# Optimization experiments

Hardware: AMD Instinct MI355X
Metric: run time of the kernel (lower is better)

## Reference

```python
import jax, jax.numpy as jnp
import numpy as np

# Model constants (match init_kwargs + mamba_ssm defaults)
CIN, COUT, K, STRIDE = 64, 128, 4, 4
D = 128            # d_model = features_out
DI = 256           # d_inner = 2*D (expand=2)
NSTATE = 16        # d_state
DCONV = 4          # depthwise conv width
DT_RANK = 8        # ceil(D/16)
NB = 3             # blocks per direction
NTOT = 2 * NB      # forward + backward stacks


def setup_inputs() -> dict:
    key = jax.random.key(0)
    ks = jax.random.split(key, 10)
    s = 0.02
    x = jax.random.normal(ks[0], (2, CIN, 8192), jnp.float32)
    convd_w = jax.random.normal(ks[1], (COUT, CIN, K), jnp.float32) * s
    convd_b = jnp.zeros((COUT,), jnp.float32)
    ln_w = jnp.ones((NTOT, D), jnp.float32)
    ln_b = jnp.zeros((NTOT, D), jnp.float32)
    in_proj_w = jax.random.normal(ks[2], (NTOT, 2 * DI, D), jnp.float32) * s
    conv_w = jax.random.normal(ks[3], (NTOT, DI, DCONV), jnp.float32) * s
    conv_b = jnp.zeros((NTOT, DI), jnp.float32)
    xproj_w = jax.random.normal(ks[4], (NTOT, DT_RANK + 2 * NSTATE, DI), jnp.float32) * s
    dtproj_w = jax.random.normal(ks[5], (NTOT, DI, DT_RANK), jnp.float32) * s
    dtproj_b = jax.random.normal(ks[6], (NTOT, DI), jnp.float32) * s
    # S4D-real init: A = -[1..N]
    A_log = jnp.log(jnp.broadcast_to(jnp.arange(1, NSTATE + 1, dtype=jnp.float32), (NTOT, DI, NSTATE)))
    Dparam = jnp.ones((NTOT, DI), jnp.float32)
    outproj_w = jax.random.normal(ks[7], (NTOT, D, DI), jnp.float32) * s
    return dict(x=x, convd_w=convd_w, convd_b=convd_b, ln_w=ln_w, ln_b=ln_b,
                in_proj_w=in_proj_w, conv_w=conv_w, conv_b=conv_b, xproj_w=xproj_w,
                dtproj_w=dtproj_w, dtproj_b=dtproj_b, A_log=A_log, Dparam=Dparam,
                outproj_w=outproj_w)


def _silu(x):
    return x * jax.nn.sigmoid(x)


def _layernorm(x, w, b, eps=1e-5):
    m = x.mean(-1, keepdims=True)
    xc = x - m
    v = (xc * xc).mean(-1, keepdims=True)
    return xc * jax.lax.rsqrt(v + eps) * w + b


def _mamba_mixer(x, in_proj_w, conv_w, conv_b, xproj_w, dtproj_w, dtproj_b, A_log, Dp, outproj_w):
    # x: (B, L, D)
    B, L, _ = x.shape
    xz = jnp.einsum('bld,ed->ble', x, in_proj_w)          # (B, L, 2*DI)
    xm, z = jnp.split(xz, 2, axis=-1)
    # causal depthwise conv (pad left DCONV-1, truncate to L)
    xp = jnp.pad(xm, ((0, 0), (DCONV - 1, 0), (0, 0)))
    xc = conv_b
    acc = jnp.zeros_like(xm)
    for k in range(DCONV):
        acc = acc + xp[:, k:k + L, :] * conv_w[:, k]
    xc = _silu(acc + conv_b)                               # (B, L, DI)
    dbc = jnp.einsum('ble,ne->bln', xc, xproj_w)           # (B, L, DT_RANK + 2N)
    dt, Bc, Cc = jnp.split(dbc, [DT_RANK, DT_RANK + NSTATE], axis=-1)
    dt = jax.nn.softplus(jnp.einsum('blr,dr->bld', dt, dtproj_w) + dtproj_b)  # (B, L, DI)
    A = -jnp.exp(A_log)                                    # (DI, N)
    dA = jnp.exp(dt[..., None] * A)                        # (B, L, DI, N)
    dBx = dt[..., None] * Bc[:, :, None, :] * xc[..., None]

    def step(h, inp):
        dA_t, dBx_t, C_t = inp
        h = dA_t * h + dBx_t                               # (B, DI, N)
        y = jnp.einsum('bdn,bn->bd', h, C_t)
        return h, y

    h0 = jnp.zeros((B, DI, NSTATE), x.dtype)
    _, ys = jax.lax.scan(step, h0, (jnp.swapaxes(dA, 0, 1), jnp.swapaxes(dBx, 0, 1), jnp.swapaxes(Cc, 0, 1)))
    y = jnp.swapaxes(ys, 0, 1)                             # (B, L, DI)
    y = (y + Dp * xc) * _silu(z)
    return jnp.einsum('ble,de->bld', y, outproj_w)         # (B, L, D)


def _mamba_stack(x, off, ln_w, ln_b, in_proj_w, conv_w, conv_b, xproj_w, dtproj_w, dtproj_b, A_log, Dparam, outproj_w):
    # mamba_ssm Block semantics: residual = x (+ prev residual); x = mixer(norm(residual))
    res = None
    cur = x
    for i in range(NB):
        j = off + i
        res = cur if res is None else cur + res
        hn = _layernorm(res, ln_w[j], ln_b[j])
        cur = _mamba_mixer(hn, in_proj_w[j], conv_w[j], conv_b[j], xproj_w[j],
                           dtproj_w[j], dtproj_b[j], A_log[j], Dparam[j], outproj_w[j])
    return cur, res


def reference(x, convd_w, convd_b, ln_w, ln_b, in_proj_w, conv_w, conv_b, xproj_w,
              dtproj_w, dtproj_b, A_log, Dparam, outproj_w):
    # downsampling conv + SiLU
    y = jax.lax.conv_general_dilated(x, convd_w, (STRIDE,), 'VALID',
                                     dimension_numbers=('NCH', 'OIH', 'NCH'))
    y = _silu(y + convd_b[None, :, None])                  # (B, COUT, L')
    h = jnp.swapaxes(y, 1, 2)                              # (B, L', D)
    xf, rf = _mamba_stack(h, 0, ln_w, ln_b, in_proj_w, conv_w, conv_b, xproj_w,
                          dtproj_w, dtproj_b, A_log, Dparam, outproj_w)
    xb, rb = _mamba_stack(h[:, ::-1, :], NB, ln_w, ln_b, in_proj_w, conv_w, conv_b, xproj_w,
                          dtproj_w, dtproj_b, A_log, Dparam, outproj_w)
    out = (xf + rf) + (xb + rb)[:, ::-1, :]
    return jnp.swapaxes(out, 1, 2), rf, rb
```

## Files before the change

### kernel.cpp

```cpp
#include <hip/hip_runtime.h>
#include <math.h>

#define B    2
#define CIN  64
#define LIN  8192
#define L    2048
#define D    128
#define DI   256
#define NS   16
#define RK   8
#define NSTREAM 4
#define CH   32
#define NCH  (L/CH)
#define TOK  (NSTREAM*L)
#define SZ_D ((size_t)TOK*D)
#define SZ_DI ((size_t)TOK*DI)
#define SXM 280
#define SHN 152

typedef short  bfrag __attribute__((ext_vector_type(8)));
typedef float  facc  __attribute__((ext_vector_type(4)));
#define MFMA __builtin_amdgcn_mfma_f32_16x16x32_bf16

__device__ __forceinline__ float sigmoidf_(float x){ return 1.f/(1.f+__expf(-x)); }
__device__ __forceinline__ float siluf_(float x){ return x*sigmoidf_(x); }
__device__ __forceinline__ ushort f2bf(float f){
    unsigned u = __float_as_uint(f);
    u += 0x7fffu + ((u>>16)&1u);
    return (ushort)(u>>16);
}
__device__ __forceinline__ float bf2f(ushort u){ return __uint_as_float(((unsigned)u)<<16); }
__device__ __forceinline__ float softplusf_(float t){
    return (t > 20.f) ? t : __logf(1.f + __expf(t));
}

__global__ void __launch_bounds__(256,1)
k_downcvt(const float* __restrict__ x, const float* __restrict__ convd_w,
          const float* __restrict__ bias,
          const float* __restrict__ ipw, const float* __restrict__ opw,
          const float* __restrict__ xpw,
          float* __restrict__ h, ushort* __restrict__ wall){
    int tid = threadIdx.x;
    if (blockIdx.x >= 128){
        int g = (blockIdx.x - 128)*256 + tid;
        for (int i = g; i < 688128; i += 32768){
// ... 30 lines not shown
    __syncthreads();
    int w = tid>>6, lane = tid&63, rw = w>>1, cw_ = w&1;
    int q = lane>>4, r = lane&15;
    int n0 = nb*64 + cw_*32;
    facc acc[2][2] = {};
    #pragma unroll
    for (int kb=0; kb<8; ++kb){
        bfrag a0 = *(bfrag*)&sxd[(rw*32 + r)*SXM + kb*32 + q*8];
        bfrag a1 = *(bfrag*)&sxd[(rw*32 + 16 + r)*SXM + kb*32 + q*8];
        bfrag b0 = *(bfrag*)&swt[(cw_*32 + r)*SXM + kb*32 + q*8];
        bfrag b1 = *(bfrag*)&swt[(cw_*32 + 16 + r)*SXM + kb*32 + q*8];
        acc[0][0] = MFMA(a0,b0,acc[0][0],0,0,0);
        acc[0][1] = MFMA(a0,b1,acc[0][1],0,0,0);
        acc[1][0] = MFMA(a1,b0,acc[1][0],0,0,0);
        acc[1][1] = MFMA(a1,b1,acc[1][1],0,0,0);
    }
    #pragma unroll
    for (int im=0; im<2; ++im)
    #pragma unroll
    for (int in=0; in<2; ++in){
        int col = n0 + in*16 + r;
        float bv = bias[col];
        #pragma unroll
        for (int r2=0; r2<4; ++r2){
            int row = m0 + rw*32 + im*16 + q*4 + r2;
            int bb = row >> 11, l = row & 2047;
            float v = siluf_(acc[im][in][r2] + bv);
            h[((size_t)(bb*L + l))*D + col] = v;
            h[((size_t)((2+bb)*L + (L-1-l)))*D + col] = v;
        }
    }
}

__global__ void __launch_bounds__(512,1)
k_head(const float* __restrict__ curIn, const float* __restrict__ resIn,
       float* __restrict__ resOut,
       const float* __restrict__ lnw, const float* __restrict__ lnb,
       const ushort* __restrict__ wbi, const ushort* __restrict__ wbx,
       const float* __restrict__ cw, const float* __restrict__ cb,
       const float* __restrict__ Wdt, const float* __restrict__ bdt,
       const float* __restrict__ A_log,
       ushort* __restrict__ zh, ushort* __restrict__ xch,
       float* __restrict__ dtr, float* __restrict__ Bc, float* __restrict__ Cc,
       float* __restrict__ Aprod, float* __restrict__ Bend, int blk, int first){
    __shared__ ushort smHn[35*SHN];
    __shared__ ushort smXm[35*SXM];
    __shared__ ushort smXc[32*SXM];
    __shared__ float  smDbc[32*68];
    const int tid = threadIdx.x;
    const int bi = blockIdx.x;
    const int s = bi >> 6, c = bi & 63;
    const int j = (s>>1)*3 + blk;
    const int base_tok = s*L + c*CH;

    {
        int t = tid >> 4, g = tid & 15;
        size_t off = (size_t)(base_tok + t)*D + g*8;
        float4 v[2];
        const float4* cp = (const float4*)(curIn + off);
        v[0] = cp[0]; v[1] = cp[1];
        if (!first){
            const float4* rp = (const float4*)(resIn + off);
            #pragma unroll
            for (int i=0;i<2;++i){ float4 rv=rp[i]; v[i].x+=rv.x; v[i].y+=rv.y; v[i].z+=rv.z; v[i].w+=rv.w; }
        }
        {
            float4* ro = (float4*)(resOut + off);
            ro[0] = v[0]; ro[1] = v[1];
        }
        float s1=0.f, s2=0.f;
        #pragma unroll
        for (int i=0;i<2;++i){
            s1 += v[i].x+v[i].y+v[i].z+v[i].w;
            s2 += v[i].x*v[i].x+v[i].y*v[i].y+v[i].z*v[i].z+v[i].w*v[i].w;
        }
        s1 += __shfl_xor(s1,1); s2 += __shfl_xor(s2,1);
        s1 += __shfl_xor(s1,2); s2 += __shfl_xor(s2,2);
        s1 += __shfl_xor(s1,4); s2 += __shfl_xor(s2,4);
        s1 += __shfl_xor(s1,8); s2 += __shfl_xor(s2,8);
        float mean = s1*(1.f/128.f);
        float var  = s2*(1.f/128.f) - mean*mean;
        float rstd = rsqrtf(var + 1e-5f);
        const float4* lwp = (const float4*)(lnw + j*D + g*8);
        const float4* lbp = (const float4*)(lnb + j*D + g*8);
        #pragma unroll
        for (int i=0;i<2;++i){
            float4 lw = lwp[i], lb = lbp[i];
            ushort4 o;
            o.x = f2bf((v[i].x-mean)*rstd*lw.x + lb.x);
            o.y = f2bf((v[i].y-mean)*rstd*lw.y + lb.y);
            o.z = f2bf((v[i].z-mean)*rstd*lw.z + lb.z);
            o.w = f2bf((v[i].w-mean)*rstd*lw.w + lb.w);
            *(ushort4*)&smHn[t*SHN + g*8 + i*4] = o;
        }
    }
    if (c > 0 && tid < 48){
        int t = tid >> 4, g = tid & 15;
        size_t off = (size_t)(base_tok - 3 + t)*D + g*8;
        float4 v[2];
        const float4* cp = (const float4*)(curIn + off);
        v[0] = cp[0]; v[1] = cp[1];
        if (!first){
            const float4* rp = (const float4*)(resIn + off);
            #pragma unroll
            for (int i=0;i<2;++i){ float4 rv=rp[i]; v[i].x+=rv.x; v[i].y+=rv.y; v[i].z+=rv.z; v[i].w+=rv.w; }
        }
        float s1=0.f, s2=0.f;
        #pragma unroll
        for (int i=0;i<2;++i){
            s1 += v[i].x+v[i].y+v[i].z+v[i].w;
            s2 += v[i].x*v[i].x+v[i].y*v[i].y+v[i].z*v[i].z+v[i].w*v[i].w;
        }
        s1 += __shfl_xor(s1,1); s2 += __shfl_xor(s2,1);
        s1 += __shfl_xor(s1,2); s2 += __shfl_xor(s2,2);
        s1 += __shfl_xor(s1,4); s2 += __shfl_xor(s2,4);
        s1 += __shfl_xor(s1,8); s2 += __shfl_xor(s2,8);
        float mean = s1*(1.f/128.f);
        float var  = s2*(1.f/128.f) - mean*mean;
        float rstd = rsqrtf(var + 1e-5f);
        const float4* lwp = (const float4*)(lnw + j*D + g*8);
        const float4* lbp = (const float4*)(lnb + j*D + g*8);
        #pragma unroll
        for (int i=0;i<2;++i){
            float4 lw = lwp[i], lb = lbp[i];
            ushort4 o;
            o.x = f2bf((v[i].x-mean)*rstd*lw.x + lb.x);
            o.y = f2bf((v[i].y-mean)*rstd*lw.y + lb.y);
            o.z = f2bf((v[i].z-mean)*rstd*lw.z + lb.z);
            o.w = f2bf((v[i].w-mean)*rstd*lw.w + lb.w);
            *(ushort4*)&smHn[(32+t)*SHN + g*8 + i*4] = o;
        }
    }
    __syncthreads();

    {
        int w = tid>>6, lane = tid&63, q = lane>>4, r = lane&15;
        bfrag a[3][4];
        #pragma unroll
        for (int rt=0; rt<3; ++rt)
        #pragma unroll
        for (int kb=0; kb<4; ++kb)
            a[rt][kb] = *(bfrag*)&smHn[(rt*16 + r)*SHN + kb*32 + q*8];
        #pragma unroll
        for (int ct=0; ct<4; ++ct){
            int n0 = w*64 + ct*16;
            const ushort* bp = wbi + ((size_t)j*512 + n0 + r)*128 + q*8;
            facc a0 = {}, a1 = {}, a2 = {};
            #pragma unroll
            for (int kb=0; kb<4; ++kb){
                bfrag bv = *(const bfrag*)(bp + kb*32);
                a0 = MFMA(a[0][kb], bv, a0, 0,0,0);
                a1 = MFMA(a[1][kb], bv, a1, 0,0,0);
                a2 = MFMA(a[2][kb], bv, a2, 0,0,0);
            }
            int colL = n0 + r;
            if (colL < DI){
                #pragma unroll
                for (int r2=0;r2<4;++r2){
                    int rr = q*4 + r2;
                    smXm[rr*SXM + colL]      = f2bf(a0[r2]);
                    smXm[(16+rr)*SXM + colL] = f2bf(a1[r2]);
                    if (rr < 3) smXm[(32+rr)*SXM + colL] = f2bf(a2[r2]);
                }
            } else {
                int cz = colL - DI;
                #pragma unroll
                for (int r2=0;r2<4;++r2){
                    int rr = q*4 + r2;
                    zh[(size_t)(base_tok + rr)*DI + cz]      = f2bf(a0[r2]);
                    zh[(size_t)(base_tok + 16 + rr)*DI + cz] = f2bf(a1[r2]);
                }
            }
        }
    }
    __syncthreads();

    {
        int d = tid & 255, th = tid >> 8;
        const float* w4 = cw + ((size_t)j*DI + d)*4;
        float cw0=w4[0], cw1=w4[1], cw2=w4[2], cw3=w4[3];
        float cbb = cb[j*DI + d];
        float xm1, xm2, xm3;
        if (th == 0){
            xm1 = xm2 = xm3 = 0.f;
            if (c > 0){
                xm3 = bf2f(smXm[32*SXM + d]);
                xm2 = bf2f(smXm[33*SXM + d]);
                xm1 = bf2f(smXm[34*SXM + d]);
            }
        } else {
            xm3 = bf2f(smXm[13*SXM + d]);
            xm2 = bf2f(smXm[14*SXM + d]);
            xm1 = bf2f(smXm[15*SXM + d]);
        }
        int l0 = th*16;
        #pragma unroll 4
        for (int i=0;i<16;++i){
            int l = l0 + i;
            float x0 = bf2f(smXm[l*SXM + d]);
            float v = siluf_(cbb + cw3*x0 + cw2*xm1 + cw1*xm2 + cw0*xm3);
            ushort vb = f2bf(v);
            smXc[l*SXM + d] = vb;
            xch[(size_t)(base_tok+l)*DI + d] = vb;
            xm3 = xm2; xm2 = xm1; xm1 = x0;
        }
    }
    __syncthreads();

    if (tid < 256){
        int w = tid>>6, lane = tid&63, q = lane>>4, r = lane&15;
        facc a0 = {}, a1 = {};
        const ushort* bp = wbx + ((size_t)j*64 + w*16 + r)*256 + q*8;
        #pragma unroll
        for (int kb=0; kb<8; ++kb){
            bfrag av0 = *(bfrag*)&smXc[r*SXM + kb*32 + q*8];
            bfrag av1 = *(bfrag*)&smXc[(16+r)*SXM + kb*32 + q*8];
            bfrag bv  = *(const bfrag*)(bp + kb*32);
            a0 = MFMA(av0, bv, a0, 0,0,0);
            a1 = MFMA(av1, bv, a1, 0,0,0);
        }
        int col = w*16 + r;
        #pragma unroll
        for (int r2=0;r2<4;++r2){
            int rr = q*4 + r2;
            smDbc[rr*68 + col]      = a0[r2];
            smDbc[(16+rr)*68 + col] = a1[r2];
            int row0 = base_tok + rr, row1 = base_tok + 16 + rr;
            if      (col < 8){  dtr[(size_t)row0*RK + col] = a0[r2];      dtr[(size_t)row1*RK + col] = a1[r2]; }
            else if (col < 24){ Bc [(size_t)row0*NS + (col-8)] = a0[r2];  Bc [(size_t)row1*NS + (col-8)] = a1[r2]; }
            else if (col < 40){ Cc [(size_t)row0*NS + (col-24)] = a0[r2]; Cc [(size_t)row1*NS + (col-24)] = a1[r2]; }
        }
    }
    __syncthreads();

    {
        int d = tid & 255, hh = tid >> 8;
        float A[8], wv[RK];
        const float* ar = A_log + ((size_t)j*DI + d)*NS + hh*8;
        #pragma unroll
        for (int n=0;n<8;++n) A[n] = -__expf(ar[n]);
        const float* wr = Wdt + ((size_t)j*DI + d)*RK;
        #pragma unroll
        for (int r=0;r<RK;++r) wv[r] = wr[r];
        float bb2 = bdt[j*DI + d];
        float ap[8], hs[8];
        #pragma unroll
        for (int n=0;n<8;++n){ ap[n]=1.f; hs[n]=0.f; }
        #pragma unroll 4
        for (int l=0;l<CH;++l){
            float t = bb2;
            #pragma unroll
            for (int r=0;r<RK;++r) t += smDbc[l*68+r]*wv[r];
            float dtv = softplusf_(t);
            float xv  = bf2f(smXc[l*SXM + d]);
            float dbx = dtv*xv;
            #pragma unroll
            for (int n=0;n<8;++n){
                float dA = __expf(dtv*A[n]);
                ap[n] *= dA;
                hs[n] = dA*hs[n] + dbx*smDbc[l*68+8+hh*8+n];
            }
        }
        size_t pb = (size_t)bi*4096 + (size_t)d*16 + hh*8;
        #pragma unroll
        for (int k4=0;k4<2;++k4){
            float4 av, bv;
            av.x=ap[k4*4+0]; av.y=ap[k4*4+1]; av.z=ap[k4*4+2]; av.w=ap[k4*4+3];
            bv.x=hs[k4*4+0]; bv.y=hs[k4*4+1]; bv.z=hs[k4*4+2]; bv.w=hs[k4*4+3];
            *(float4*)&Aprod[pb + k4*4] = av;
            *(float4*)&Bend [pb + k4*4] = bv;
        }
    }
}

__global__ void k_scanmid(const float* __restrict__ Aprod, float* __restrict__ Bend){
    int tid = blockIdx.x*128 + threadIdx.x;
    int s = tid >> 12;
    int nd = tid & 4095;
    size_t base = (size_t)s*NCH*4096 + nd;
    float h = 0.f;
    for (int c0=0; c0<NCH; c0+=16){
        float a[16], b[16];
        #pragma unroll
        for (int i=0;i<16;++i){
            a[i] = Aprod[base + (size_t)(c0+i)*4096];
            b[i] = Bend [base + (size_t)(c0+i)*4096];
        }
        #pragma unroll
        for (int i=0;i<16;++i){
            Bend[base + (size_t)(c0+i)*4096] = h;
            h = a[i]*h + b[i];
        }
    }
}

__global__ void __launch_bounds__(512,1)
k_tail(const float* __restrict__ dtr, const ushort* __restrict__ xch,
       const float* __restrict__ Bc, const float* __restrict__ Cc,
       const float* __restrict__ A_log,
       const float* __restrict__ Wdt, const float* __restrict__ bdt,
       const float* __restrict__ h0, const ushort* __restrict__ zh,
       const float* __restrict__ Dp, const ushort* __restrict__ wbo,
       float* __restrict__ cur, int blk){
    int c = blockIdx.x, s = blockIdx.y; int j = (s>>1)*3 + blk;
    int tid = threadIdx.x;
    __shared__ float sB[CH*NS], sC[CH*NS], sdtr[CH*RK];
    __shared__ ushort sg[CH*SXM];
    int base_tok = s*L + c*CH;
    sB[tid] = Bc[(size_t)base_tok*NS + tid];
    sC[tid] = Cc[(size_t)base_tok*NS + tid];
    if (tid < 256) sdtr[tid] = dtr[(size_t)base_tok*RK + tid];
    int d = tid >> 1, hh = tid & 1;
    float A[8], wv[RK];
    const float* ar = A_log + ((size_t)j*DI + d)*NS + hh*8;
    #pragma unroll
    for (int n=0;n<8;++n) A[n] = -__expf(ar[n]);
    const float* wr = Wdt + ((size_t)j*DI + d)*RK;
    #pragma unroll
    for (int r=0;r<RK;++r) wv[r] = wr[r];
    float bb = bdt[j*DI + d];
    float Dpd = Dp[j*DI + d];
    float hs[8];
    {
        size_t pb = (size_t)(s*NCH + c)*4096 + (size_t)d*16 + hh*8;
        float4 h0v0 = *(const float4*)&h0[pb];
        float4 h0v1 = *(const float4*)&h0[pb+4];
        hs[0]=h0v0.x; hs[1]=h0v0.y; hs[2]=h0v0.z; hs[3]=h0v0.w;
        hs[4]=h0v1.x; hs[5]=h0v1.y; hs[6]=h0v1.z; hs[7]=h0v1.w;
    }
    __syncthreads();
    #pragma unroll 4
    for (int l=0;l<CH;++l){
        float t = bb;
        #pragma unroll
        for (int r=0;r<RK;++r) t += sdtr[l*RK+r]*wv[r];
        float dtv = softplusf_(t);
        float xv  = bf2f(xch[(size_t)(base_tok+l)*DI + d]);
        float dbx = dtv*xv;
        float p = 0.f;
        #pragma unroll
        for (int n=0;n<8;++n){
            float dA = __expf(dtv*A[n]);
            hs[n] = dA*hs[n] + dbx*sB[l*NS+hh*8+n];
            p += hs[n]*sC[l*NS+hh*8+n];
        }
        p += __shfl_xor(p, 1);
        if (hh == 0){
            float zv = bf2f(zh[(size_t)(base_tok+l)*DI + d]);
            sg[l*SXM + d] = f2bf((p + Dpd*xv)*siluf_(zv));
        }
    }
    __syncthreads();
    int w = tid>>6, lane = tid&63, q = lane>>4, r = lane&15;
    facc acc0 = {}, acc1 = {};
    const ushort* b0p = wbo + ((size_t)j*128 + w*16 + r)*256 + q*8;
    #pragma unroll
    for (int kb=0; kb<8; ++kb){
        bfrag av0 = *(bfrag*)&sg[r*SXM + kb*32 + q*8];
        bfrag av1 = *(bfrag*)&sg[(16+r)*SXM + kb*32 + q*8];
        bfrag bv0 = *(const bfrag*)(b0p + kb*32);
        acc0 = MFMA(av0,bv0,acc0,0,0,0);
        acc1 = MFMA(av1,bv0,acc1,0,0,0);
    }
    int col = w*16 + r;
    #pragma unroll
    for (int r2=0;r2<4;++r2){
        int row0 = base_tok + q*4 + r2;
        cur[(size_t)row0*D + col]      = acc0[r2];
        cur[(size_t)(row0+16)*D + col] = acc1[r2];
    }
}

__global__ void k_final(const float* __restrict__ cur, const float* __restrict__ res,
                        float* __restrict__ out){
    int l = blockIdx.x, b = blockIdx.y, d = threadIdx.x;
    int tf = (b*L + l)*D + d;
    int tbk = ((2+b)*L + (L-1-l))*D + d;
    float f  = cur[tf] + res[tf];
    float bw = cur[tbk] + res[tbk];
    out[((size_t)(b*D + d))*L + l] = f + bw;
    out[(size_t)2*D*L + (size_t)(b*L + l)*D + d] = res[tf];
    out[(size_t)2*D*L + (size_t)((2+b)*L + l)*D + d] = res[((2+b)*L + l)*D + d];
}

extern "C" void kernel_launch(void* const* d_in, const int* in_sizes, int n_in,
                              void* d_out, int out_size, void* d_ws, size_t ws_size,
                              hipStream_t stream){
    const float* x         = (const float*)d_in[0];
    const float* convd_w   = (const float*)d_in[1];
    const float* convd_b   = (const float*)d_in[2];
    const float* ln_w      = (const float*)d_in[3];
    const float* ln_b      = (const float*)d_in[4];
    const float* in_proj_w = (const float*)d_in[5];
    const float* conv_w    = (const float*)d_in[6];
    const float* conv_b    = (const float*)d_in[7];
    const float* xproj_w   = (const float*)d_in[8];
    const float* dtproj_w  = (const float*)d_in[9];
    const float* dtproj_b  = (const float*)d_in[10];
    const float* A_log     = (const float*)d_in[11];
    const float* Dparam    = (const float*)d_in[12];
    const float* outproj_w = (const float*)d_in[13];

    float* ws = (float*)d_ws;
    float* h     = ws; ws += SZ_D;
    float* res0  = ws; ws += SZ_D;
    float* res1  = ws; ws += SZ_D;
    float* cur   = ws; ws += SZ_D;
    ushort* zh   = (ushort*)ws; ws += SZ_DI/2;
    ushort* xch  = (ushort*)ws; ws += SZ_DI/2;
    float* Aprod = ws; ws += SZ_D;
    float* Bend  = ws; ws += SZ_D;
    float* dtr   = ws; ws += (size_t)TOK*RK;
    float* Bc    = ws; ws += (size_t)TOK*NS;
    float* Cc    = ws; ws += (size_t)TOK*NS;
    ushort* wall = (ushort*)ws;
    ushort* wbi  = wall;
    ushort* wbo  = wall + 393216;
    ushort* wbx  = wall + 589824;

    k_downcvt<<<256, 256, 0, stream>>>(x, convd_w, convd_b, in_proj_w, outproj_w,
                                       xproj_w, h, wall);

    float* resin[3]  = { nullptr, res0, res1 };
    float* resout[3] = { res0,    res1, res0 };
    for (int blk = 0; blk < 3; ++blk){
        const float* ci = (blk==0) ? h : cur;
        const float* ri = (blk==0) ? h : resin[blk];
        k_head<<<NSTREAM*NCH, 512, 0, stream>>>(ci, ri, resout[blk], ln_w, ln_b, wbi, wbx,
                                                conv_w, conv_b, dtproj_w, dtproj_b, A_log,
                                                zh, xch, dtr, Bc, Cc, Aprod, Bend, blk, blk==0);
        k_scanmid<<<128, 128, 0, stream>>>(Aprod, Bend);
        k_tail<<<dim3(NCH, NSTREAM), 512, 0, stream>>>(dtr, xch, Bc, Cc, A_log,
                                                       dtproj_w, dtproj_b, Bend, zh,
                                                       Dparam, wbo, cur, blk);
    }

    k_final<<<dim3(L, B), 128, 0, stream>>>(cur, res0, (float*)d_out);
}
```

Baseline: 264.8 us.

## Fuse head, chunk scan and tail into one kernel with inter-block lookback flags

Merges the per-layer head, mid-scan and tail kernels into a single kernel where each chunk block publishes its chunk-local decay product and end state, waits on flags for earlier chunks, and serially combines their prefixes to get its initial state. This removes two launches per layer and the global round trips for xc, dt, B and C intermediates, keeping them in shared memory. It relies on all blocks being co-resident for the spin-wait and adds a lookback whose cost grows with the chunk index. The final output kernel also transposes through shared memory for coalesced stores.

After: 351.8 us. 32.8% more time.

```diff
diff --git a/kernel.cpp b/kernel.cpp
--- a/kernel.cpp
+++ b/kernel.cpp
@@ -108,22 +108,26 @@
 }
 
 __global__ void __launch_bounds__(512,1)
-k_head(const float* __restrict__ curIn, const float* __restrict__ resIn,
-       float* __restrict__ resOut,
-       const float* __restrict__ lnw, const float* __restrict__ lnb,
-       const ushort* __restrict__ wbi, const ushort* __restrict__ wbx,
-       const float* __restrict__ cw, const float* __restrict__ cb,
-       const float* __restrict__ Wdt, const float* __restrict__ bdt,
-       const float* __restrict__ A_log,
-       ushort* __restrict__ zh, ushort* __restrict__ xch,
-       float* __restrict__ dtr, float* __restrict__ Bc, float* __restrict__ Cc,
-       float* __restrict__ Aprod, float* __restrict__ Bend, int blk, int first){
-    __shared__ ushort smHn[35*SHN];
-    __shared__ ushort smXm[35*SXM];
-    __shared__ ushort smXc[32*SXM];
-    __shared__ float  smDbc[32*68];
+k_layer(const float* __restrict__ curIn, const float* __restrict__ resIn,
+        float* __restrict__ resOut, float* __restrict__ curOut,
+        const float* __restrict__ lnw, const float* __restrict__ lnb,
+        const ushort* __restrict__ wbi, const ushort* __restrict__ wbx,
+        const ushort* __restrict__ wbo,
+        const float* __restrict__ cw, const float* __restrict__ cb,
+        const float* __restrict__ Wdt, const float* __restrict__ bdt,
+        const float* __restrict__ A_log, const float* __restrict__ Dp,
+        ushort* __restrict__ zh,
+        float* __restrict__ Ap, float* __restrict__ Bp,
+        unsigned* __restrict__ fl, int blk, int first){
+    __shared__ __align__(16) char smem[56864];
+    ushort* smHn  = (ushort*)smem;
+    ushort* smXm  = (ushort*)(smem + 10640);
+    ushort* smXc  = (ushort*)(smem + 30240);
+    float*  smDbc = (float*) (smem + 48160);
+    ushort* sg    = (ushort*)smem;
+
     const int tid = threadIdx.x;
-    const int bi = blockIdx.x;
+    const int bi  = blockIdx.x;
     const int s = bi >> 6, c = bi & 63;
     const int j = (s>>1)*3 + blk;
     const int base_tok = s*L + c*CH;
@@ -274,9 +278,7 @@
             int l = l0 + i;
             float x0 = bf2f(smXm[l*SXM + d]);
             float v = siluf_(cbb + cw3*x0 + cw2*xm1 + cw1*xm2 + cw0*xm3);
-            ushort vb = f2bf(v);
-            smXc[l*SXM + d] = vb;
-            xch[(size_t)(base_tok+l)*DI + d] = vb;
+            smXc[l*SXM + d] = f2bf(v);
             xm3 = xm2; xm2 = xm1; xm1 = x0;
         }
     }
@@ -300,162 +302,173 @@
             int rr = q*4 + r2;
             smDbc[rr*68 + col]      = a0[r2];
             smDbc[(16+rr)*68 + col] = a1[r2];
-            int row0 = base_tok + rr, row1 = base_tok + 16 + rr;
-            if      (col < 8){  dtr[(size_t)row0*RK + col] = a0[r2];      dtr[(size_t)row1*RK + col] = a1[r2]; }
-            else if (col < 24){ Bc [(size_t)row0*NS + (col-8)] = a0[r2];  Bc [(size_t)row1*NS + (col-8)] = a1[r2]; }
-            else if (col < 40){ Cc [(size_t)row0*NS + (col-24)] = a0[r2]; Cc [(size_t)row1*NS + (col-24)] = a1[r2]; }
-        }
-    }
-    __syncthreads();
-
-    {
-        int d = tid & 255, hh = tid >> 8;
-        float A[8], wv[RK];
-        const float* ar = A_log + ((size_t)j*DI + d)*NS + hh*8;
-        #pragma unroll
-        for (int n=0;n<8;++n) A[n] = -__expf(ar[n]);
-        const float* wr = Wdt + ((size_t)j*DI + d)*RK;
+        }
+    }
+    __syncthreads();
+
+    const int d2 = tid >> 1, hh = tid & 1;
+    float A8[8], wv[RK];
+    {
+        const float* ar = A_log + ((size_t)j*DI + d2)*NS + hh*8;
+        #pragma unroll
+        for (int n=0;n<8;++n) A8[n] = -__expf(ar[n]);
+        const float* wr = Wdt + ((size_t)j*DI + d2)*RK;
         #pragma unroll
         for (int r=0;r<RK;++r) wv[r] = wr[r];
-        float bb2 = bdt[j*DI + d];
-        float ap[8], hs[8];
-        #pragma unroll
-        for (int n=0;n<8;++n){ ap[n]=1.f; hs[n]=0.f; }
+    }
+    const float bb2 = bdt[j*DI + d2];
+
+    {
+        float ap[8], hsv[8];
+        #pragma unroll
+        for (int n=0;n<8;++n){ ap[n]=1.f; hsv[n]=0.f; }
         #pragma unroll 4
         for (int l=0;l<CH;++l){
             float t = bb2;
             #pragma unroll
             for (int r=0;r<RK;++r) t += smDbc[l*68+r]*wv[r];
             float dtv = softplusf_(t);
-            float xv  = bf2f(smXc[l*SXM + d]);
+            float xv  = bf2f(smXc[l*SXM + d2]);
             float dbx = dtv*xv;
             #pragma unroll
             for (int n=0;n<8;++n){
-                float dA = __expf(dtv*A[n]);
+                float dA = __expf(dtv*A8[n]);
                 ap[n] *= dA;
+                hsv[n] = dA*hsv[n] + dbx*smDbc[l*68+8+hh*8+n];
+            }
+        }
+        size_t pb = (size_t)bi*4096 + (size_t)d2*16 + hh*8;
+        float4 av0, av1, bv0, bv1;
+        av0.x=ap[0];av0.y=ap[1];av0.z=ap[2];av0.w=ap[3];
+        av1.x=ap[4];av1.y=ap[5];av1.z=ap[6];av1.w=ap[7];
+        bv0.x=hsv[0];bv0.y=hsv[1];bv0.z=hsv[2];bv0.w=hsv[3];
+        bv1.x=hsv[4];bv1.y=hsv[5];bv1.z=hsv[6];bv1.w=hsv[7];
+        *(float4*)&Ap[pb]   = av0; *(float4*)&Ap[pb+4] = av1;
+        *(float4*)&Bp[pb]   = bv0; *(float4*)&Bp[pb+4] = bv1;
+    }
+    __syncthreads();
+    if (tid == 0){
+        __threadfence();
+        __hip_atomic_store(&fl[bi], 1u, __ATOMIC_RELEASE, __HIP_MEMORY_SCOPE_AGENT);
+    }
+    if (tid < 64 && c > 0){
+        const unsigned* fp = fl + s*64 + tid;
+        bool ok = (tid >= c);
+        unsigned guard = 0;
+        while (true){
+            if (!ok) ok = (__hip_atomic_load(fp, __ATOMIC_ACQUIRE, __HIP_MEMORY_SCOPE_AGENT) != 0);
+            if (__all(ok)) break;
+            __builtin_amdgcn_s_sleep(2);
+            if (++guard > 20000000u) break;
+        }
+    }
+    __syncthreads();
+
+    float hs[8];
+    #pragma unroll
+    for (int n=0;n<8;++n) hs[n] = 0.f;
+    {
+        size_t sb = ((size_t)(s*64))*4096 + (size_t)d2*16 + hh*8;
+        int ci = 0;
+        for (; ci+4 <= c; ci += 4){
+            float4 aa[4][2], bb4[4][2];
+            #pragma unroll
+            for (int u=0;u<4;++u){
+                const float4* av = (const float4*)&Ap[sb + (size_t)(ci+u)*4096];
+                const float4* bv = (const float4*)&Bp[sb + (size_t)(ci+u)*4096];
+                aa[u][0]=av[0]; aa[u][1]=av[1]; bb4[u][0]=bv[0]; bb4[u][1]=bv[1];
+            }
+            #pragma unroll
+            for (int u=0;u<4;++u){
+                hs[0]=aa[u][0].x*hs[0]+bb4[u][0].x; hs[1]=aa[u][0].y*hs[1]+bb4[u][0].y;
+                hs[2]=aa[u][0].z*hs[2]+bb4[u][0].z; hs[3]=aa[u][0].w*hs[3]+bb4[u][0].w;
+                hs[4]=aa[u][1].x*hs[4]+bb4[u][1].x; hs[5]=aa[u][1].y*hs[5]+bb4[u][1].y;
+                hs[6]=aa[u][1].z*hs[6]+bb4[u][1].z; hs[7]=aa[u][1].w*hs[7]+bb4[u][1].w;
+            }
+        }
+        for (; ci < c; ++ci){
+            const float4* av = (const float4*)&Ap[sb + (size_t)ci*4096];
+            const float4* bv = (const float4*)&Bp[sb + (size_t)ci*4096];
+            float4 a0=av[0], a1=av[1], b0=bv[0], b1=bv[1];
+            hs[0]=a0.x*hs[0]+b0.x; hs[1]=a0.y*hs[1]+b0.y;
+            hs[2]=a0.z*hs[2]+b0.z; hs[3]=a0.w*hs[3]+b0.w;
+            hs[4]=a1.x*hs[4]+b1.x; hs[5]=a1.y*hs[5]+b1.y;
+            hs[6]=a1.z*hs[6]+b1.z; hs[7]=a1.w*hs[7]+b1.w;
+        }
+    }
+
+    {
+        float Dpd = Dp[j*DI + d2];
+        #pragma unroll 4
+        for (int l=0;l<CH;++l){
+            float t = bb2;
+            #pragma unroll
+            for (int r=0;r<RK;++r) t += smDbc[l*68+r]*wv[r];
+            float dtv = softplusf_(t);
+            float xv  = bf2f(smXc[l*SXM + d2]);
+            float dbx = dtv*xv;
+            float p = 0.f;
+            #pragma unroll
+            for (int n=0;n<8;++n){
+                float dA = __expf(dtv*A8[n]);
                 hs[n] = dA*hs[n] + dbx*smDbc[l*68+8+hh*8+n];
-            }
-        }
-        size_t pb = (size_t)bi*4096 + (size_t)d*16 + hh*8;
-        #pragma unroll
-        for (int k4=0;k4<2;++k4){
-            float4 av, bv;
-            av.x=ap[k4*4+0]; av.y=ap[k4*4+1]; av.z=ap[k4*4+2]; av.w=ap[k4*4+3];
-            bv.x=hs[k4*4+0]; bv.y=hs[k4*4+1]; bv.z=hs[k4*4+2]; bv.w=hs[k4*4+3];
-            *(float4*)&Aprod[pb + k4*4] = av;
-            *(float4*)&Bend [pb + k4*4] = bv;
+                p += hs[n]*smDbc[l*68+24+hh*8+n];
+            }
+            p += __shfl_xor(p, 1);
+            if (hh == 0){
+                float zv = bf2f(zh[(size_t)(base_tok+l)*DI + d2]);
+                sg[l*SXM + d2] = f2bf((p + Dpd*xv)*siluf_(zv));
+            }
+        }
+    }
+    __syncthreads();
+
+    {
+        int w = tid>>6, lane = tid&63, q = lane>>4, r = lane&15;
+        facc acc0 = {}, acc1 = {};
+        const ushort* b0p = wbo + ((size_t)j*128 + w*16 + r)*256 + q*8;
+        #pragma unroll
+        for (int kb=0; kb<8; ++kb){
+            bfrag av0 = *(bfrag*)&sg[r*SXM + kb*32 + q*8];
+            bfrag av1 = *(bfrag*)&sg[(16+r)*SXM + kb*32 + q*8];
+            bfrag bv0 = *(const bfrag*)(b0p + kb*32);
+            acc0 = MFMA(av0,bv0,acc0,0,0,0);
+            acc1 = MFMA(av1,bv0,acc1,0,0,0);
+        }
+        int col = w*16 + r;
+        #pragma unroll
+        for (int r2=0;r2<4;++r2){
+            int row0 = base_tok + q*4 + r2;
+            curOut[(size_t)row0*D + col]      = acc0[r2];
+            curOut[(size_t)(row0+16)*D + col] = acc1[r2];
         }
     }
 }
 
-__global__ void k_scanmid(const float* __restrict__ Aprod, float* __restrict__ Bend){
-    int tid = blockIdx.x*128 + threadIdx.x;
-    int s = tid >> 12;
-    int nd = tid & 4095;
-    size_t base = (size_t)s*NCH*4096 + nd;
-    float h = 0.f;
-    for (int c0=0; c0<NCH; c0+=16){
-        float a[16], b[16];
-        #pragma unroll
-        for (int i=0;i<16;++i){
-            a[i] = Aprod[base + (size_t)(c0+i)*4096];
-            b[i] = Bend [base + (size_t)(c0+i)*4096];
-        }
-        #pragma unroll
-        for (int i=0;i<16;++i){
-            Bend[base + (size_t)(c0+i)*4096] = h;
-            h = a[i]*h + b[i];
-        }
-    }
-}
-
-__global__ void __launch_bounds__(512,1)
-k_tail(const float* __restrict__ dtr, const ushort* __restrict__ xch,
-       const float* __restrict__ Bc, const float* __restrict__ Cc,
-       const float* __restrict__ A_log,
-       const float* __restrict__ Wdt, const float* __restrict__ bdt,
-       const float* __restrict__ h0, const ushort* __restrict__ zh,
-       const float* __restrict__ Dp, const ushort* __restrict__ wbo,
-       float* __restrict__ cur, int blk){
-    int c = blockIdx.x, s = blockIdx.y; int j = (s>>1)*3 + blk;
+__global__ void __launch_bounds__(256,1)
+k_final(const float* __restrict__ cur, const float* __restrict__ res,
+        float* __restrict__ out){
+    __shared__ float sf[128*33];
+    int b = blockIdx.y, l0 = blockIdx.x*32;
     int tid = threadIdx.x;
-    __shared__ float sB[CH*NS], sC[CH*NS], sdtr[CH*RK];
-    __shared__ ushort sg[CH*SXM];
-    int base_tok = s*L + c*CH;
-    sB[tid] = Bc[(size_t)base_tok*NS + tid];
-    sC[tid] = Cc[(size_t)base_tok*NS + tid];
-    if (tid < 256) sdtr[tid] = dtr[(size_t)base_tok*RK + tid];
-    int d = tid >> 1, hh = tid & 1;
-    float A[8], wv[RK];
-    const float* ar = A_log + ((size_t)j*DI + d)*NS + hh*8;
     #pragma unroll
-    for (int n=0;n<8;++n) A[n] = -__expf(ar[n]);
-    const float* wr = Wdt + ((size_t)j*DI + d)*RK;
+    for (int k=0;k<16;++k){
+        int idx = tid + k*256;
+        int l = l0 + (idx>>7), d = idx&127;
+        int tf  = (b*L + l)*D + d;
+        int tbk = ((2+b)*L + (L-1-l))*D + d;
+        float f = cur[tf] + res[tf] + cur[tbk] + res[tbk];
+        sf[d*33 + (l-l0)] = f;
+        out[(size_t)2*D*L + tf] = res[tf];
+        out[(size_t)2*D*L + (size_t)((2+b)*L + l)*D + d] = res[((2+b)*L + l)*D + d];
+    }
+    __syncthreads();
     #pragma unroll
-    for (int r=0;r<RK;++r) wv[r] = wr[r];
-    float bb = bdt[j*DI + d];
-    float Dpd = Dp[j*DI + d];
-    float hs[8];
-    {
-        size_t pb = (size_t)(s*NCH + c)*4096 + (size_t)d*16 + hh*8;
-        float4 h0v0 = *(const float4*)&h0[pb];
-        float4 h0v1 = *(const float4*)&h0[pb+4];
-        hs[0]=h0v0.x; hs[1]=h0v0.y; hs[2]=h0v0.z; hs[3]=h0v0.w;
-        hs[4]=h0v1.x; hs[5]=h0v1.y; hs[6]=h0v1.z; hs[7]=h0v1.w;
-    }
-    __syncthreads();
-    #pragma unroll 4
-    for (int l=0;l<CH;++l){
-        float t = bb;
-        #pragma unroll
-        for (int r=0;r<RK;++r) t += sdtr[l*RK+r]*wv[r];
-        float dtv = softplusf_(t);
-        float xv  = bf2f(xch[(size_t)(base_tok+l)*DI + d]);
-        float dbx = dtv*xv;
-        float p = 0.f;
-        #pragma unroll
-        for (int n=0;n<8;++n){
-            float dA = __expf(dtv*A[n]);
-            hs[n] = dA*hs[n] + dbx*sB[l*NS+hh*8+n];
-            p += hs[n]*sC[l*NS+hh*8+n];
-        }
-        p += __shfl_xor(p, 1);
-        if (hh == 0){
-            float zv = bf2f(zh[(size_t)(base_tok+l)*DI + d]);
-            sg[l*SXM + d] = f2bf((p + Dpd*xv)*siluf_(zv));
-        }
-    }
-    __syncthreads();
-    int w = tid>>6, lane = tid&63, q = lane>>4, r = lane&15;
-    facc acc0 = {}, acc1 = {};
-    const ushort* b0p = wbo + ((size_t)j*128 + w*16 + r)*256 + q*8;
-    #pragma unroll
-    for (int kb=0; kb<8; ++kb){
-        bfrag av0 = *(bfrag*)&sg[r*SXM + kb*32 + q*8];
-        bfrag av1 = *(bfrag*)&sg[(16+r)*SXM + kb*32 + q*8];
-        bfrag bv0 = *(const bfrag*)(b0p + kb*32);
-        acc0 = MFMA(av0,bv0,acc0,0,0,0);
-        acc1 = MFMA(av1,bv0,acc1,0,0,0);
-    }
-    int col = w*16 + r;
-    #pragma unroll
-    for (int r2=0;r2<4;++r2){
-        int row0 = base_tok + q*4 + r2;
-        cur[(size_t)row0*D + col]      = acc0[r2];
-        cur[(size_t)(row0+16)*D + col] = acc1[r2];
-    }
-}
-
-__global__ void k_final(const float* __restrict__ cur, const float* __restrict__ res,
-                        float* __restrict__ out){
-    int l = blockIdx.x, b = blockIdx.y, d = threadIdx.x;
-    int tf = (b*L + l)*D + d;
-    int tbk = ((2+b)*L + (L-1-l))*D + d;
-    float f  = cur[tf] + res[tf];
-    float bw = cur[tbk] + res[tbk];
-    out[((size_t)(b*D + d))*L + l] = f + bw;
-    out[(size_t)2*D*L + (size_t)(b*L + l)*D + d] = res[tf];
-    out[(size_t)2*D*L + (size_t)((2+b)*L + l)*D + d] = res[((2+b)*L + l)*D + d];
+    for (int k=0;k<16;++k){
+        int idx = tid + k*256;
+        int d = idx>>5, li = idx&31;
+        out[((size_t)(b*D + d))*L + l0 + li] = sf[d*33 + li];
+    }
 }
 
 extern "C" void kernel_launch(void* const* d_in, const int* in_sizes, int n_in,
@@ -480,35 +493,32 @@
     float* h     = ws; ws += SZ_D;
     float* res0  = ws; ws += SZ_D;
     float* res1  = ws; ws += SZ_D;
-    float* cur   = ws; ws += SZ_D;
+    float* cur0  = ws; ws += SZ_D;
+    float* cur1  = ws; ws += SZ_D;
     ushort* zh   = (ushort*)ws; ws += SZ_DI/2;
-    ushort* xch  = (ushort*)ws; ws += SZ_DI/2;
-    float* Aprod = ws; ws += SZ_D;
-    float* Bend  = ws; ws += SZ_D;
-    float* dtr   = ws; ws += (size_t)TOK*RK;
-    float* Bc    = ws; ws += (size_t)TOK*NS;
-    float* Cc    = ws; ws += (size_t)TOK*NS;
+    float* Ap    = ws; ws += SZ_D;
+    float* Bp    = ws; ws += SZ_D;
+    unsigned* flags = (unsigned*)ws; ws += 768;
     ushort* wall = (ushort*)ws;
     ushort* wbi  = wall;
     ushort* wbo  = wall + 393216;
     ushort* wbx  = wall + 589824;
 
+    hipMemsetAsync((void*)flags, 0, 3072, stream);
     k_downcvt<<<256, 256, 0, stream>>>(x, convd_w, convd_b, in_proj_w, outproj_w,
                                        xproj_w, h, wall);
 
-    float* resin[3]  = { nullptr, res0, res1 };
-    float* resout[3] = { res0,    res1, res0 };
+    const float* ci[3] = { h,    cur0, cur1 };
+    const float* ri[3] = { h,    res0, res1 };
+    float*       ro[3] = { res0, res1, res0 };
+    float*       co[3] = { cur0, cur1, cur0 };
     for (int blk = 0; blk < 3; ++blk){
-        const float* ci = (blk==0) ? h : cur;
-        const float* ri = (blk==0) ? h : resin[blk];
-        k_head<<<NSTREAM*NCH, 512, 0, stream>>>(ci, ri, resout[blk], ln_w, ln_b, wbi, wbx,
-                                                conv_w, conv_b, dtproj_w, dtproj_b, A_log,
-                                                zh, xch, dtr, Bc, Cc, Aprod, Bend, blk, blk==0);
-        k_scanmid<<<128, 128, 0, stream>>>(Aprod, Bend);
-        k_tail<<<dim3(NCH, NSTREAM), 512, 0, stream>>>(dtr, xch, Bc, Cc, A_log,
-                                                       dtproj_w, dtproj_b, Bend, zh,
-                                                       Dparam, wbo, cur, blk);
-    }
-
-    k_final<<<dim3(L, B), 128, 0, stream>>>(cur, res0, (float*)d_out);
+        k_layer<<<NSTREAM*NCH, 512, 0, stream>>>(ci[blk], ri[blk], ro[blk], co[blk],
+                                                 ln_w, ln_b, wbi, wbx, wbo,
+                                                 conv_w, conv_b, dtproj_w, dtproj_b,
+                                                 A_log, Dparam, zh, Ap, Bp,
+                                                 flags + blk*256, blk, blk==0);
+    }
+
+    k_final<<<dim3(NCH, B), 256, 0, stream>>>(cur0, res0, (float*)d_out);
 }
```

## Halve scan chunk size to double block count and rewrite final transpose

Applied to the files above, without the earlier changes.

Reduces the per-block chunk from 32 to 16 tokens, so twice as many blocks are launched for the head and tail kernels, and raises launch bounds so several blocks can share a CU. Index maps, shared buffers, MFMA tiles and the Aprod/Bend workspace sizes are rescaled to match. The final kernel now transposes through shared memory so its stores are coalesced. In exchange, the inter-chunk scan has twice as many chunk states to combine, each MFMA call does less work, and halo recomputation grows relative to the work per block.

After: 274.4 us. 3.6% more time.

```diff
diff --git a/kernel.cpp b/kernel.cpp
--- a/kernel.cpp
+++ b/kernel.cpp
@@ -10,7 +10,7 @@
 #define NS   16
 #define RK   8
 #define NSTREAM 4
-#define CH   32
+#define CH   16
 #define NCH  (L/CH)
 #define TOK  (NSTREAM*L)
 #define SZ_D ((size_t)TOK*D)
@@ -107,7 +107,7 @@
     }
 }
 
-__global__ void __launch_bounds__(512,1)
+__global__ void __launch_bounds__(512,4)
 k_head(const float* __restrict__ curIn, const float* __restrict__ resIn,
        float* __restrict__ resOut,
        const float* __restrict__ lnw, const float* __restrict__ lnb,
@@ -118,101 +118,78 @@
        ushort* __restrict__ zh, ushort* __restrict__ xch,
        float* __restrict__ dtr, float* __restrict__ Bc, float* __restrict__ Cc,
        float* __restrict__ Aprod, float* __restrict__ Bend, int blk, int first){
-    __shared__ ushort smHn[35*SHN];
-    __shared__ ushort smXm[35*SXM];
-    __shared__ ushort smXc[32*SXM];
-    __shared__ float  smDbc[32*68];
+    __shared__ ushort smHn[32*SHN];
+    __shared__ ushort smXm[19*SXM];
+    __shared__ ushort smXc[16*SXM];
+    __shared__ float  smDbc[16*68];
     const int tid = threadIdx.x;
     const int bi = blockIdx.x;
-    const int s = bi >> 6, c = bi & 63;
+    const int s = bi >> 7, c = bi & 127;
     const int j = (s>>1)*3 + blk;
     const int base_tok = s*L + c*CH;
 
     {
-        int t = tid >> 4, g = tid & 15;
-        size_t off = (size_t)(base_tok + t)*D + g*8;
-        float4 v[2];
-        const float4* cp = (const float4*)(curIn + off);
-        v[0] = cp[0]; v[1] = cp[1];
+        int t = tid >> 5, g = tid & 31;
+        size_t off = (size_t)(base_tok + t)*D + g*4;
+        float4 v = *(const float4*)(curIn + off);
         if (!first){
-            const float4* rp = (const float4*)(resIn + off);
-            #pragma unroll
-            for (int i=0;i<2;++i){ float4 rv=rp[i]; v[i].x+=rv.x; v[i].y+=rv.y; v[i].z+=rv.z; v[i].w+=rv.w; }
-        }
-        {
-            float4* ro = (float4*)(resOut + off);
-            ro[0] = v[0]; ro[1] = v[1];
-        }
-        float s1=0.f, s2=0.f;
-        #pragma unroll
-        for (int i=0;i<2;++i){
-            s1 += v[i].x+v[i].y+v[i].z+v[i].w;
-            s2 += v[i].x*v[i].x+v[i].y*v[i].y+v[i].z*v[i].z+v[i].w*v[i].w;
-        }
-        s1 += __shfl_xor(s1,1); s2 += __shfl_xor(s2,1);
-        s1 += __shfl_xor(s1,2); s2 += __shfl_xor(s2,2);
-        s1 += __shfl_xor(s1,4); s2 += __shfl_xor(s2,4);
-        s1 += __shfl_xor(s1,8); s2 += __shfl_xor(s2,8);
+            float4 rv = *(const float4*)(resIn + off);
+            v.x+=rv.x; v.y+=rv.y; v.z+=rv.z; v.w+=rv.w;
+        }
+        *(float4*)(resOut + off) = v;
+        float s1 = v.x+v.y+v.z+v.w;
+        float s2 = v.x*v.x+v.y*v.y+v.z*v.z+v.w*v.w;
+        s1 += __shfl_xor(s1,1);  s2 += __shfl_xor(s2,1);
+        s1 += __shfl_xor(s1,2);  s2 += __shfl_xor(s2,2);
+        s1 += __shfl_xor(s1,4);  s2 += __shfl_xor(s2,4);
+        s1 += __shfl_xor(s1,8);  s2 += __shfl_xor(s2,8);
+        s1 += __shfl_xor(s1,16); s2 += __shfl_xor(s2,16);
         float mean = s1*(1.f/128.f);
         float var  = s2*(1.f/128.f) - mean*mean;
         float rstd = rsqrtf(var + 1e-5f);
-        const float4* lwp = (const float4*)(lnw + j*D + g*8);
-        const float4* lbp = (const float4*)(lnb + j*D + g*8);
-        #pragma unroll
-        for (int i=0;i<2;++i){
-            float4 lw = lwp[i], lb = lbp[i];
-            ushort4 o;
-            o.x = f2bf((v[i].x-mean)*rstd*lw.x + lb.x);
-            o.y = f2bf((v[i].y-mean)*rstd*lw.y + lb.y);
-            o.z = f2bf((v[i].z-mean)*rstd*lw.z + lb.z);
-            o.w = f2bf((v[i].w-mean)*rstd*lw.w + lb.w);
-            *(ushort4*)&smHn[t*SHN + g*8 + i*4] = o;
-        }
-    }
-    if (c > 0 && tid < 48){
-        int t = tid >> 4, g = tid & 15;
-        size_t off = (size_t)(base_tok - 3 + t)*D + g*8;
-        float4 v[2];
-        const float4* cp = (const float4*)(curIn + off);
-        v[0] = cp[0]; v[1] = cp[1];
+        float4 lw = *(const float4*)(lnw + j*D + g*4);
+        float4 lb = *(const float4*)(lnb + j*D + g*4);
+        ushort4 o;
+        o.x = f2bf((v.x-mean)*rstd*lw.x + lb.x);
+        o.y = f2bf((v.y-mean)*rstd*lw.y + lb.y);
+        o.z = f2bf((v.z-mean)*rstd*lw.z + lb.z);
+        o.w = f2bf((v.w-mean)*rstd*lw.w + lb.w);
+        *(ushort4*)&smHn[t*SHN + g*4] = o;
+    }
+    if (c > 0 && tid < 96){
+        int t = tid >> 5, g = tid & 31;
+        size_t off = (size_t)(base_tok - 3 + t)*D + g*4;
+        float4 v = *(const float4*)(curIn + off);
         if (!first){
-            const float4* rp = (const float4*)(resIn + off);
-            #pragma unroll
-            for (int i=0;i<2;++i){ float4 rv=rp[i]; v[i].x+=rv.x; v[i].y+=rv.y; v[i].z+=rv.z; v[i].w+=rv.w; }
-        }
-        float s1=0.f, s2=0.f;
-        #pragma unroll
-        for (int i=0;i<2;++i){
-            s1 += v[i].x+v[i].y+v[i].z+v[i].w;
-            s2 += v[i].x*v[i].x+v[i].y*v[i].y+v[i].z*v[i].z+v[i].w*v[i].w;
-        }
-        s1 += __shfl_xor(s1,1); s2 += __shfl_xor(s2,1);
-        s1 += __shfl_xor(s1,2); s2 += __shfl_xor(s2,2);
-        s1 += __shfl_xor(s1,4); s2 += __shfl_xor(s2,4);
-        s1 += __shfl_xor(s1,8); s2 += __shfl_xor(s2,8);
+            float4 rv = *(const float4*)(resIn + off);
+            v.x+=rv.x; v.y+=rv.y; v.z+=rv.z; v.w+=rv.w;
+        }
+        float s1 = v.x+v.y+v.z+v.w;
+        float s2 = v.x*v.x+v.y*v.y+v.z*v.z+v.w*v.w;
+        s1 += __shfl_xor(s1,1);  s2 += __shfl_xor(s2,1);
+        s1 += __shfl_xor(s1,2);  s2 += __shfl_xor(s2,2);
+        s1 += __shfl_xor(s1,4);  s2 += __shfl_xor(s2,4);
+        s1 += __shfl_xor(s1,8);  s2 += __shfl_xor(s2,8);
+        s1 += __shfl_xor(s1,16); s2 += __shfl_xor(s2,16);
         float mean = s1*(1.f/128.f);
         float var  = s2*(1.f/128.f) - mean*mean;
         float rstd = rsqrtf(var + 1e-5f);
-        const float4* lwp = (const float4*)(lnw + j*D + g*8);
-        const float4* lbp = (const float4*)(lnb + j*D + g*8);
-        #pragma unroll
-        for (int i=0;i<2;++i){
-            float4 lw = lwp[i], lb = lbp[i];
-            ushort4 o;
-            o.x = f2bf((v[i].x-mean)*rstd*lw.x + lb.x);
-            o.y = f2bf((v[i].y-mean)*rstd*lw.y + lb.y);
-            o.z = f2bf((v[i].z-mean)*rstd*lw.z + lb.z);
-            o.w = f2bf((v[i].w-mean)*rstd*lw.w + lb.w);
-            *(ushort4*)&smHn[(32+t)*SHN + g*8 + i*4] = o;
-        }
+        float4 lw = *(const float4*)(lnw + j*D + g*4);
+        float4 lb = *(const float4*)(lnb + j*D + g*4);
+        ushort4 o;
+        o.x = f2bf((v.x-mean)*rstd*lw.x + lb.x);
+        o.y = f2bf((v.y-mean)*rstd*lw.y + lb.y);
+        o.z = f2bf((v.z-mean)*rstd*lw.z + lb.z);
+        o.w = f2bf((v.w-mean)*rstd*lw.w + lb.w);
+        *(ushort4*)&smHn[(16+t)*SHN + g*4] = o;
     }
     __syncthreads();
 
     {
         int w = tid>>6, lane = tid&63, q = lane>>4, r = lane&15;
-        bfrag a[3][4];
-        #pragma unroll
-        for (int rt=0; rt<3; ++rt)
+        bfrag a[2][4];
+        #pragma unroll
+        for (int rt=0; rt<2; ++rt)
         #pragma unroll
         for (int kb=0; kb<4; ++kb)
             a[rt][kb] = *(bfrag*)&smHn[(rt*16 + r)*SHN + kb*32 + q*8];
@@ -220,30 +197,27 @@
         for (int ct=0; ct<4; ++ct){
             int n0 = w*64 + ct*16;
             const ushort* bp = wbi + ((size_t)j*512 + n0 + r)*128 + q*8;
-            facc a0 = {}, a1 = {}, a2 = {};
+            facc a0 = {}, a1 = {};
             #pragma unroll
             for (int kb=0; kb<4; ++kb){
                 bfrag bv = *(const bfrag*)(bp + kb*32);
                 a0 = MFMA(a[0][kb], bv, a0, 0,0,0);
                 a1 = MFMA(a[1][kb], bv, a1, 0,0,0);
-                a2 = MFMA(a[2][kb], bv, a2, 0,0,0);
             }
             int colL = n0 + r;
             if (colL < DI){
                 #pragma unroll
                 for (int r2=0;r2<4;++r2){
                     int rr = q*4 + r2;
-                    smXm[rr*SXM + colL]      = f2bf(a0[r2]);
-                    smXm[(16+rr)*SXM + colL] = f2bf(a1[r2]);
-                    if (rr < 3) smXm[(32+rr)*SXM + colL] = f2bf(a2[r2]);
+                    smXm[rr*SXM + colL] = f2bf(a0[r2]);
+                    if (rr < 3) smXm[(16+rr)*SXM + colL] = f2bf(a1[r2]);
                 }
             } else {
                 int cz = colL - DI;
                 #pragma unroll
                 for (int r2=0;r2<4;++r2){
                     int rr = q*4 + r2;
-                    zh[(size_t)(base_tok + rr)*DI + cz]      = f2bf(a0[r2]);
-                    zh[(size_t)(base_tok + 16 + rr)*DI + cz] = f2bf(a1[r2]);
+                    zh[(size_t)(base_tok + rr)*DI + cz] = f2bf(a0[r2]);
                 }
             }
         }
@@ -259,18 +233,18 @@
         if (th == 0){
             xm1 = xm2 = xm3 = 0.f;
             if (c > 0){
-                xm3 = bf2f(smXm[32*SXM + d]);
-                xm2 = bf2f(smXm[33*SXM + d]);
-                xm1 = bf2f(smXm[34*SXM + d]);
+                xm3 = bf2f(smXm[16*SXM + d]);
+                xm2 = bf2f(smXm[17*SXM + d]);
+                xm1 = bf2f(smXm[18*SXM + d]);
             }
         } else {
-            xm3 = bf2f(smXm[13*SXM + d]);
-            xm2 = bf2f(smXm[14*SXM + d]);
-            xm1 = bf2f(smXm[15*SXM + d]);
-        }
-        int l0 = th*16;
-        #pragma unroll 4
-        for (int i=0;i<16;++i){
+            xm3 = bf2f(smXm[5*SXM + d]);
+            xm2 = bf2f(smXm[6*SXM + d]);
+            xm1 = bf2f(smXm[7*SXM + d]);
+        }
+        int l0 = th*8;
+        #pragma unroll
+        for (int i=0;i<8;++i){
             int l = l0 + i;
             float x0 = bf2f(smXm[l*SXM + d]);
             float v = siluf_(cbb + cw3*x0 + cw2*xm1 + cw1*xm2 + cw0*xm3);
@@ -284,32 +258,29 @@
 
     if (tid < 256){
         int w = tid>>6, lane = tid&63, q = lane>>4, r = lane&15;
-        facc a0 = {}, a1 = {};
+        facc a0 = {};
         const ushort* bp = wbx + ((size_t)j*64 + w*16 + r)*256 + q*8;
         #pragma unroll
         for (int kb=0; kb<8; ++kb){
             bfrag av0 = *(bfrag*)&smXc[r*SXM + kb*32 + q*8];
-            bfrag av1 = *(bfrag*)&smXc[(16+r)*SXM + kb*32 + q*8];
             bfrag bv  = *(const bfrag*)(bp + kb*32);
             a0 = MFMA(av0, bv, a0, 0,0,0);
-            a1 = MFMA(av1, bv, a1, 0,0,0);
         }
         int col = w*16 + r;
         #pragma unroll
         for (int r2=0;r2<4;++r2){
             int rr = q*4 + r2;
-            smDbc[rr*68 + col]      = a0[r2];
-            smDbc[(16+rr)*68 + col] = a1[r2];
-            int row0 = base_tok + rr, row1 = base_tok + 16 + rr;
-            if      (col < 8){  dtr[(size_t)row0*RK + col] = a0[r2];      dtr[(size_t)row1*RK + col] = a1[r2]; }
-            else if (col < 24){ Bc [(size_t)row0*NS + (col-8)] = a0[r2];  Bc [(size_t)row1*NS + (col-8)] = a1[r2]; }
-            else if (col < 40){ Cc [(size_t)row0*NS + (col-24)] = a0[r2]; Cc [(size_t)row1*NS + (col-24)] = a1[r2]; }
+            smDbc[rr*68 + col] = a0[r2];
+            int row0 = base_tok + rr;
+            if      (col < 8){  dtr[(size_t)row0*RK + col] = a0[r2]; }
+            else if (col < 24){ Bc [(size_t)row0*NS + (col-8)] = a0[r2]; }
+            else if (col < 40){ Cc [(size_t)row0*NS + (col-24)] = a0[r2]; }
         }
     }
     __syncthreads();
 
     {
-        int d = tid & 255, hh = tid >> 8;
+        int d = tid >> 1, hh = tid & 1;
         float A[8], wv[RK];
         const float* ar = A_log + ((size_t)j*DI + d)*NS + hh*8;
         #pragma unroll
@@ -337,14 +308,15 @@
             }
         }
         size_t pb = (size_t)bi*4096 + (size_t)d*16 + hh*8;
-        #pragma unroll
-        for (int k4=0;k4<2;++k4){
-            float4 av, bv;
-            av.x=ap[k4*4+0]; av.y=ap[k4*4+1]; av.z=ap[k4*4+2]; av.w=ap[k4*4+3];
-            bv.x=hs[k4*4+0]; bv.y=hs[k4*4+1]; bv.z=hs[k4*4+2]; bv.w=hs[k4*4+3];
-            *(float4*)&Aprod[pb + k4*4] = av;
-            *(float4*)&Bend [pb + k4*4] = bv;
-        }
+        float4 av0, bv0;
+        av0.x=ap[0];av0.y=ap[1];av0.z=ap[2];av0.w=ap[3];
+        bv0.x=hs[0];bv0.y=hs[1];bv0.z=hs[2];bv0.w=hs[3];
+        *(float4*)&Aprod[pb]   = av0;
+        *(float4*)&Bend [pb]   = bv0;
+        av0.x=ap[4];av0.y=ap[5];av0.z=ap[6];av0.w=ap[7];
+        bv0.x=hs[4];bv0.y=hs[5];bv0.z=hs[6];bv0.w=hs[7];
+        *(float4*)&Aprod[pb+4] = av0;
+        *(float4*)&Bend [pb+4] = bv0;
     }
 }
 
@@ -369,7 +341,7 @@
     }
 }
 
-__global__ void __launch_bounds__(512,1)
+__global__ void __launch_bounds__(512,4)
 k_tail(const float* __restrict__ dtr, const ushort* __restrict__ xch,
        const float* __restrict__ Bc, const float* __restrict__ Cc,
        const float* __restrict__ A_log,
@@ -382,9 +354,11 @@
     __shared__ float sB[CH*NS], sC[CH*NS], sdtr[CH*RK];
     __shared__ ushort sg[CH*SXM];
     int base_tok = s*L + c*CH;
-    sB[tid] = Bc[(size_t)base_tok*NS + tid];
-    sC[tid] = Cc[(size_t)base_tok*NS + tid];
-    if (tid < 256) sdtr[tid] = dtr[(size_t)base_tok*RK + tid];
+    if (tid < 256){
+        sB[tid] = Bc[(size_t)base_tok*NS + tid];
+        sC[tid] = Cc[(size_t)base_tok*NS + tid];
+    }
+    if (tid < 128) sdtr[tid] = dtr[(size_t)base_tok*RK + tid];
     int d = tid >> 1, hh = tid & 1;
     float A[8], wv[RK];
     const float* ar = A_log + ((size_t)j*DI + d)*NS + hh*8;
@@ -427,35 +401,46 @@
     }
     __syncthreads();
     int w = tid>>6, lane = tid&63, q = lane>>4, r = lane&15;
-    facc acc0 = {}, acc1 = {};
+    facc acc0 = {};
     const ushort* b0p = wbo + ((size_t)j*128 + w*16 + r)*256 + q*8;
     #pragma unroll
     for (int kb=0; kb<8; ++kb){
         bfrag av0 = *(bfrag*)&sg[r*SXM + kb*32 + q*8];
-        bfrag av1 = *(bfrag*)&sg[(16+r)*SXM + kb*32 + q*8];
         bfrag bv0 = *(const bfrag*)(b0p + kb*32);
         acc0 = MFMA(av0,bv0,acc0,0,0,0);
-        acc1 = MFMA(av1,bv0,acc1,0,0,0);
     }
     int col = w*16 + r;
     #pragma unroll
     for (int r2=0;r2<4;++r2){
         int row0 = base_tok + q*4 + r2;
-        cur[(size_t)row0*D + col]      = acc0[r2];
-        cur[(size_t)(row0+16)*D + col] = acc1[r2];
-    }
-}
-
-__global__ void k_final(const float* __restrict__ cur, const float* __restrict__ res,
-                        float* __restrict__ out){
-    int l = blockIdx.x, b = blockIdx.y, d = threadIdx.x;
-    int tf = (b*L + l)*D + d;
-    int tbk = ((2+b)*L + (L-1-l))*D + d;
-    float f  = cur[tf] + res[tf];
-    float bw = cur[tbk] + res[tbk];
-    out[((size_t)(b*D + d))*L + l] = f + bw;
-    out[(size_t)2*D*L + (size_t)(b*L + l)*D + d] = res[tf];
-    out[(size_t)2*D*L + (size_t)((2+b)*L + l)*D + d] = res[((2+b)*L + l)*D + d];
+        cur[(size_t)row0*D + col] = acc0[r2];
+    }
+}
+
+__global__ void __launch_bounds__(256,1)
+k_final(const float* __restrict__ cur, const float* __restrict__ res,
+        float* __restrict__ out){
+    __shared__ float sf[128*33];
+    int b = blockIdx.y, l0 = blockIdx.x*32;
+    int tid = threadIdx.x;
+    #pragma unroll
+    for (int k=0;k<16;++k){
+        int idx = tid + k*256;
+        int l = l0 + (idx>>7), d = idx&127;
+        int tf  = (b*L + l)*D + d;
+        int tbk = ((2+b)*L + (L-1-l))*D + d;
+        float f = cur[tf] + res[tf] + cur[tbk] + res[tbk];
+        sf[d*33 + (l-l0)] = f;
+        out[(size_t)2*D*L + tf] = res[tf];
+        out[(size_t)2*D*L + (size_t)((2+b)*L + l)*D + d] = res[((2+b)*L + l)*D + d];
+    }
+    __syncthreads();
+    #pragma unroll
+    for (int k=0;k<16;++k){
+        int idx = tid + k*256;
+        int d = idx>>5, li = idx&31;
+        out[((size_t)(b*D + d))*L + l0 + li] = sf[d*33 + li];
+    }
 }
 
 extern "C" void kernel_launch(void* const* d_in, const int* in_sizes, int n_in,
@@ -483,8 +468,8 @@
     float* cur   = ws; ws += SZ_D;
     ushort* zh   = (ushort*)ws; ws += SZ_DI/2;
     ushort* xch  = (ushort*)ws; ws += SZ_DI/2;
-    float* Aprod = ws; ws += SZ_D;
-    float* Bend  = ws; ws += SZ_D;
+    float* Aprod = ws; ws += SZ_DI;
+    float* Bend  = ws; ws += SZ_DI;
     float* dtr   = ws; ws += (size_t)TOK*RK;
     float* Bc    = ws; ws += (size_t)TOK*NS;
     float* Cc    = ws; ws += (size_t)TOK*NS;
@@ -510,5 +495,5 @@
                                                        Dparam, wbo, cur, blk);
     }
 
-    k_final<<<dim3(L, B), 128, 0, stream>>>(cur, res0, (float*)d_out);
-}
+    k_final<<<dim3(L/32, B), 256, 0, stream>>>(cur, res0, (float*)d_out);
+}
```
